# Kernel tuning notes

Measured on AMD Instinct MI355X. Metric: run time of the kernel, lower is better.

Reference implementation:

```python
import jax, jax.numpy as jnp
import numpy as np

B = 16384          # batch
NS = 26            # sparse features
ND = 13            # dense features
V = 100000         # vocab per sparse feature
E = 16             # embedding size
H = 400            # dnn hidden
DNN_IN = NS * E + ND  # 429


def setup_inputs() -> dict:
    key = jax.random.key(0)
    ks = jax.random.split(key, 12)
    X_sparse = jax.random.randint(ks[0], (B, NS), 0, V, dtype=jnp.int32)
    X_dense = jax.random.normal(ks[1], (B, ND), dtype=jnp.float32)
    # stacked per-feature embedding tables: [NS, V, dim]
    emb1 = jax.random.normal(ks[2], (NS, V, 1), dtype=jnp.float32) * 1e-4
    emb2 = jax.random.normal(ks[3], (NS, V, E), dtype=jnp.float32) * 1e-4
    lin_weight = jax.random.normal(ks[4], (ND, 1), dtype=jnp.float32) * 1e-4
    bias = jnp.zeros((1,), dtype=jnp.float32)
    W0 = jax.random.normal(ks[5], (DNN_IN, H), dtype=jnp.float32) * 1e-4
    b0 = jnp.zeros((H,), dtype=jnp.float32)
    W1 = jax.random.normal(ks[6], (H, H), dtype=jnp.float32) * 1e-4
    b1 = jnp.zeros((H,), dtype=jnp.float32)
    W2 = jax.random.normal(ks[7], (H, H), dtype=jnp.float32) * 1e-4
    b2 = jnp.zeros((H,), dtype=jnp.float32)
    W_out = jax.random.normal(ks[8], (H, 1), dtype=jnp.float32) * 1e-4
    return {"X_sparse": X_sparse, "X_dense": X_dense, "emb1": emb1, "emb2": emb2,
            "lin_weight": lin_weight, "bias": bias, "W0": W0, "b0": b0,
            "W1": W1, "b1": b1, "W2": W2, "b2": b2, "W_out": W_out}


def reference(X_sparse, X_dense, emb1, emb2, lin_weight, bias, W0, b0, W1, b1, W2, b2, W_out):
    fidx = jnp.arange(NS)[None, :]            # [1, NS] feature indices
    # ---- FM linear term ----
    e1 = emb1[fidx, X_sparse][..., 0]          # [B, NS] per-feature scalar embeddings
    linear_sparse = jnp.sum(e1, axis=-1, keepdims=True)            # [B, 1]
    linear_dense = X_dense @ lin_weight                            # [B, 1]
    logit = linear_sparse + linear_dense
    # ---- FM second-order cross term ----
    e2 = emb2[fidx, X_sparse]                  # [B, NS, E]
    square_of_sum = jnp.square(jnp.sum(e2, axis=1))                # [B, E]
    sum_of_square = jnp.sum(jnp.square(e2), axis=1)                # [B, E]
    cross = 0.5 * jnp.sum(square_of_sum - sum_of_square, axis=-1, keepdims=True)
    logit = logit + cross
    # ---- DNN (dropout p=0 -> identity) ----
    dnn_in = jnp.concatenate([e2.reshape(e2.shape[0], -1), X_dense], axis=-1)  # [B, 429]
    h = jax.nn.relu(dnn_in @ W0 + b0)
    h = jax.nn.relu(h @ W1 + b1)
    h = jax.nn.relu(h @ W2 + b2)
    logit = logit + h @ W_out
    return logit + bias
```

## Files before the change

kernel.cpp:

```cpp
#include <hip/hip_runtime.h>
#include <hip/hip_bf16.h>

#define B_     16384
#define NS_    26
#define ND_    13
#define V_     100000
#define H_     400
#define NP     448
#define MT     64
#define ASTR   456
#define WCHB   (448 * 64)

#define ACT_OFF   0
#define WBUF_OFF  (MT * ASTR)
#define FMV_OFF   (WBUF_OFF + 2 * WCHB)
#define DOT_OFF   (FMV_OFF + 256)
#define LDSB      (DOT_OFF + 256)

#define SC_A1   2097152.0f
#define SC_A2   2147483648.0f
#define SC_F0   0.125f
#define SC_F1   0.25f
#define SC_G    1.1368683772161603e-13f

typedef float f32x4 __attribute__((ext_vector_type(4)));

__device__ __forceinline__ unsigned char f2fp8(float v) {
  int pk = __builtin_amdgcn_cvt_pk_fp8_f32(v, v, 0, false);
  return (unsigned char)(pk & 0xff);
}

__global__ __launch_bounds__(256) void prep_w(
    const float* __restrict__ W0, const float* __restrict__ W1,
    const float* __restrict__ W2, const float* __restrict__ b0,
    const float* __restrict__ b1, const float* __restrict__ b2,
    const float* __restrict__ Wout,
    unsigned char* __restrict__ W0t, unsigned char* __restrict__ W1t,
    unsigned char* __restrict__ W2t, float* __restrict__ b0p,
    float* __restrict__ b1p, float* __restrict__ b2p,
    float* __restrict__ woutp) {
  const int blk = blockIdx.x;
  const int tid = threadIdx.x;
  if (blk < 147) {
    const int layer = blk / 49;
    const int t = blk - layer * 49;
    const int k0 = (t / 7) * 64, n0 = (t - (t / 7) * 7) * 64;
    const float* W = (layer == 0) ? W0 : (layer == 1) ? W1 : W2;
    unsigned char* Wt = (layer == 0) ? W0t : (layer == 1) ? W1t : W2t;
    const int Kdim = (layer == 0) ? 429 : 400;
    __shared__ float tile[64][65];
#pragma unroll
    for (int p = 0; p < 16; ++p) {
      int kk = p * 4 + (tid >> 6);
      int k = k0 + kk;
      int n = n0 + (tid & 63);
      float v = (k < Kdim && n < H_) ? W[k * H_ + n] : 0.f;
      tile[kk][tid & 63] = v;
    }
    __syncthreads();
#pragma unroll
    for (int p = 0; p < 4; ++p) {
      int nn = p * 16 + (tid >> 4);
      int n = n0 + nn;
      int k4 = (tid & 15) * 4;
      float sc[4];
#pragma unroll
      for (int i = 0; i < 4; ++i) {
        int kabs = k0 + k4 + i;
        sc[i] = (layer == 0 && kabs >= 416) ? 262144.0f : 4096.0f;
      }
      float v0 = tile[k4 + 0][nn] * sc[0];
      float v1 = tile[k4 + 1][nn] * sc[1];
      float v2 = tile[k4 + 2][nn] * sc[2];
      float v3 = tile[k4 + 3][nn] * sc[3];
      int w = __builtin_amdgcn_cvt_pk_fp8_f32(v0, v1, 0, false);
      w = __builtin_amdgcn_cvt_pk_fp8_f32(v2, v3, w, true);
      *(unsigned int*)(Wt + (size_t)n * NP + k0 + k4) = (unsigned int)w;
    }
  } else {
    for (int it = 0; it < 7; ++it) {
      int j = it * 256 + tid;
      if (j < NP)              b0p[j]          = (j < H_) ? b0[j] * SC_A1 : 0.f;
      else if (j < 2 * NP)     b1p[j - NP]     = (j - NP < H_) ? b1[j - NP] * SC_A2 : 0.f;
      else if (j < 3 * NP)     b2p[j - 2*NP]   = (j - 2*NP < H_) ? b2[j - 2*NP] : 0.f;
      else if (j < 4 * NP)     woutp[j - 3*NP] = (j - 3*NP < H_) ? Wout[j - 3*NP] : 0.f;
    }
  }
}

__device__ __forceinline__ void stage_w_chunk(
    const unsigned char* __restrict__ Wt, int kt, unsigned char* wb,
    int wave, int lane) {
#pragma unroll
  for (int i = 0; i < 7; ++i) {
    int sbase = i * 256 + wave * 64;
    int s = sbase + lane;
    int n = s >> 2, g = s & 3;
    const unsigned char* gp = Wt + (size_t)n * NP + kt * 64 + g * 16;
    unsigned char* lp = wb + (size_t)sbase * 16;
    __builtin_amdgcn_global_load_lds(
        (const __attribute__((address_space(1))) unsigned int*)gp,
        (__attribute__((address_space(3))) unsigned int*)lp, 16, 0, 0);
  }
}

__global__ __launch_bounds__(256, 1) void fused_all(
    const int* __restrict__ Xs, const float* __restrict__ Xd,
    const float* __restrict__ emb1, const float* __restrict__ emb2,
    const float* __restrict__ linw, const float* __restrict__ bias,
    const unsigned char* __restrict__ W0t, const unsigned char* __restrict__ W1t,
    const unsigned char* __restrict__ W2t,
    const float* __restrict__ b0p, const float* __restrict__ b1p,
    const float* __restrict__ b2p, const float* __restrict__ woutp,
    float* __restrict__ out) {
  extern __shared__ char smem[];
  unsigned char* act  = (unsigned char*)(smem + ACT_OFF);
  unsigned char* wbuf = (unsigned char*)(smem + WBUF_OFF);
  float* fmv  = (float*)(smem + FMV_OFF);
  float* dotv = (float*)(smem + DOT_OFF);

  const int tid  = threadIdx.x;
  const int wave = tid >> 6;
  const int lane = tid & 63;
  const int quad = lane >> 4;
  const int l16  = lane & 15;
  const int r0   = blockIdx.x * MT;

  stage_w_chunk(W0t, 0, wbuf, wave, lane);

  {
    if (tid < 64) dotv[tid] = 0.f;
    const int r   = lane >> 2;
    const int t4  = lane & 3;
    const int row = wave * 16 + r;
    const int gr  = r0 + row;
    const int* xs = Xs + gr * NS_;

    f32x4 sum = {0.f, 0.f, 0.f, 0.f}, sq = {0.f, 0.f, 0.f, 0.f};
#pragma unroll
    for (int f = 0; f < NS_; ++f) {
      int idx = xs[f];
      f32x4 v = *(const f32x4*)(emb2 + ((size_t)f * V_ + idx) * 16 + t4 * 4);
      sum += v;
      sq  += v * v;
      int pk = __builtin_amdgcn_cvt_pk_fp8_f32(v[0] * 4096.f, v[1] * 4096.f, 0, false);
      pk = __builtin_amdgcn_cvt_pk_fp8_f32(v[2] * 4096.f, v[3] * 4096.f, pk, true);
      *(unsigned int*)(act + row * ASTR + f * 16 + t4 * 4) = (unsigned int)pk;
    }

    float lin = 0.f;
    for (int f = t4; f < NS_; f += 4)
      lin += emb1[(size_t)f * V_ + xs[f]];

    for (int e = 416 + t4; e < NP; e += 4) act[row * ASTR + e] = 0;
    for (int e = t4; e < ND_; e += 4) {
      float xd = Xd[gr * ND_ + e];
      lin += xd * linw[e];
      act[row * ASTR + 416 + e] = f2fp8(xd * 64.f);
    }

    f32x4 c4 = sum * sum - sq;
    float fm = 0.5f * (c4[0] + c4[1] + c4[2] + c4[3]) + lin;
    fm += __shfl_xor(fm, 1, 64);
    fm += __shfl_xor(fm, 2, 64);
    if (t4 == 0) fmv[row] = fm + bias[0];
  }

  const unsigned char* Wl[3] = {W0t, W1t, W2t};

  for (int layer = 0; layer < 3; ++layer) {
    f32x4 acc[4][7] = {};

    for (int kt = 0; kt < 7; ++kt) {
      __syncthreads();
      if (kt < 6)
        stage_w_chunk(Wl[layer], kt + 1, wbuf + ((kt + 1) & 1) * WCHB, wave, lane);
      const unsigned char* wb = wbuf + (kt & 1) * WCHB;

#pragma unroll
      for (int h = 0; h < 2; ++h) {
        long long av[4];
#pragma unroll
        for (int mt = 0; mt < 4; ++mt)
          av[mt] = *(const long long*)(act + (mt * 16 + l16) * ASTR + kt * 64 + h * 32 + quad * 8);
#pragma unroll
        for (int nt = 0; nt < 7; ++nt) {
          long long bv = *(const long long*)(wb + (wave * 112 + nt * 16 + l16) * 64 + h * 32 + quad * 8);
#pragma unroll
          for (int mt = 0; mt < 4; ++mt)
            acc[mt][nt] = __builtin_amdgcn_mfma_f32_16x16x32_fp8_fp8(av[mt], bv, acc[mt][nt], 0, 0, 0);
        }
      }
    }

    __syncthreads();

    if (layer < 2) {
      stage_w_chunk(Wl[layer + 1], 0, wbuf, wave, lane);
      const float fs = (layer == 0) ? SC_F0 : SC_F1;
      const float* bl = (layer == 0) ? b0p : b1p;
#pragma unroll
      for (int nt = 0; nt < 7; ++nt) {
        int col = wave * 112 + nt * 16 + l16;
        float bz = bl[col];
#pragma unroll
        for (int mt = 0; mt < 4; ++mt) {
#pragma unroll
          for (int r = 0; r < 4; ++r) {
            float v = acc[mt][nt][r] * fs + bz;
            v = v > 0.f ? v : 0.f;
            act[(mt * 16 + quad * 4 + r) * ASTR + col] = f2fp8(v);
          }
        }
      }
    } else {
      float wsum[4][4] = {};
#pragma unroll
      for (int nt = 0; nt < 7; ++nt) {
        int col = wave * 112 + nt * 16 + l16;
        float bz = b2p[col];
        float wv = woutp[col];
#pragma unroll
        for (int mt = 0; mt < 4; ++mt) {
#pragma unroll
          for (int r = 0; r < 4; ++r) {
            float v = acc[mt][nt][r] * SC_G + bz;
            v = v > 0.f ? v : 0.f;
            wsum[mt][r] += v * wv;
          }
        }
      }
#pragma unroll
      for (int mt = 0; mt < 4; ++mt) {
#pragma unroll
        for (int r = 0; r < 4; ++r) {
          float s = wsum[mt][r];
          s += __shfl_xor(s, 1, 64);
          s += __shfl_xor(s, 2, 64);
          s += __shfl_xor(s, 4, 64);
          s += __shfl_xor(s, 8, 64);
          if (l16 == 0) atomicAdd(&dotv[mt * 16 + quad * 4 + r], s);
        }
      }
    }
  }

  __syncthreads();
  if (tid < 64) out[r0 + tid] = fmv[tid] + dotv[tid];
}

extern "C" void kernel_launch(void* const* d_in, const int* in_sizes, int n_in,
                              void* d_out, int out_size, void* d_ws, size_t ws_size,
                              hipStream_t stream) {
  const int*   Xs   = (const int*)d_in[0];
  const float* Xd   = (const float*)d_in[1];
  const float* emb1 = (const float*)d_in[2];
  const float* emb2 = (const float*)d_in[3];
  const float* linw = (const float*)d_in[4];
  const float* bias = (const float*)d_in[5];
  const float* W0   = (const float*)d_in[6];
  const float* b0   = (const float*)d_in[7];
  const float* W1   = (const float*)d_in[8];
  const float* b1   = (const float*)d_in[9];
  const float* W2   = (const float*)d_in[10];
  const float* b2   = (const float*)d_in[11];
  const float* Wout = (const float*)d_in[12];
  float* out = (float*)d_out;

  char* ws = (char*)d_ws;
  const size_t WSZ = (size_t)NP * NP;
  unsigned char* W0t = (unsigned char*)(ws);
  unsigned char* W1t = (unsigned char*)(ws + WSZ);
  unsigned char* W2t = (unsigned char*)(ws + 2 * WSZ);
  float* b0p   = (float*)(ws + 3 * WSZ);
  float* b1p   = (float*)(ws + 3 * WSZ + 1792);
  float* b2p   = (float*)(ws + 3 * WSZ + 2 * 1792);
  float* woutp = (float*)(ws + 3 * WSZ + 3 * 1792);

  (void)hipFuncSetAttribute((const void*)fused_all,
                            hipFuncAttributeMaxDynamicSharedMemorySize, LDSB);

  prep_w<<<148, 256, 0, stream>>>(W0, W1, W2, b0, b1, b2, Wout,
                                  W0t, W1t, W2t, b0p, b1p, b2p, woutp);

  fused_all<<<B_ / MT, 256, LDSB, stream>>>(
      Xs, Xd, emb1, emb2, linw, bias, W0t, W1t, W2t,
      b0p, b1p, b2p, woutp, out);
}
```

Measured before the change: 284.5 us.

## Make weight staging wave-private with swizzled LDS layout and vmcnt waits

Each wave now stages only its own 112-column slice of the weight chunk into LDS, so the per-k-tile block-wide __syncthreads is replaced by s_waitcnt on vmcnt within the wave. The LDS layout of weight rows is XOR-swizzled in 16-byte groups to cut bank conflicts on the B-operand reads. Prefetch of the next layer's first chunk is issued before the layer barrier, and barriers are added around the activation rewrite. The correctness of the hard-coded waitcnt encodings and the assumption that no wave reads another's weight slice are the main risks.

After: 274.3 us. 1.04x faster.

```diff
diff --git a/kernel.cpp b/kernel.cpp
--- a/kernel.cpp
+++ b/kernel.cpp
@@ -10,12 +10,16 @@
 #define MT     64
 #define ASTR   456
 #define WCHB   (448 * 64)
+#define WQTR   (112 * 64)
 
 #define ACT_OFF   0
 #define WBUF_OFF  (MT * ASTR)
 #define FMV_OFF   (WBUF_OFF + 2 * WCHB)
 #define DOT_OFF   (FMV_OFF + 256)
 #define LDSB      (DOT_OFF + 256)
+
+#define WAIT_VM7  0x0F77
+#define WAIT_VM0  0x0F70
 
 #define SC_A1   2097152.0f
 #define SC_A2   2147483648.0f
@@ -91,13 +95,15 @@
 __device__ __forceinline__ void stage_w_chunk(
     const unsigned char* __restrict__ Wt, int kt, unsigned char* wb,
     int wave, int lane) {
+  const unsigned char* wrow = Wt + (size_t)(wave * 112) * NP + kt * 64;
+  unsigned char* lbase = wb + wave * WQTR;
 #pragma unroll
   for (int i = 0; i < 7; ++i) {
-    int sbase = i * 256 + wave * 64;
-    int s = sbase + lane;
-    int n = s >> 2, g = s & 3;
-    const unsigned char* gp = Wt + (size_t)n * NP + kt * 64 + g * 16;
-    unsigned char* lp = wb + (size_t)sbase * 16;
+    int s = i * 64 + lane;
+    int nl = s >> 2;
+    int g = (s & 3) ^ ((nl >> 1) & 3);
+    const unsigned char* gp = wrow + (size_t)nl * NP + g * 16;
+    unsigned char* lp = lbase + (size_t)(i * 64) * 16;
     __builtin_amdgcn_global_load_lds(
         (const __attribute__((address_space(1))) unsigned int*)gp,
         (__attribute__((address_space(3))) unsigned int*)lp, 16, 0, 0);
@@ -166,16 +172,24 @@
     if (t4 == 0) fmv[row] = fm + bias[0];
   }
 
+  __syncthreads();
+
   const unsigned char* Wl[3] = {W0t, W1t, W2t};
 
   for (int layer = 0; layer < 3; ++layer) {
+    const unsigned char* Wt = Wl[layer];
+    const unsigned char* wq = wbuf + wave * WQTR;
     f32x4 acc[4][7] = {};
 
     for (int kt = 0; kt < 7; ++kt) {
-      __syncthreads();
-      if (kt < 6)
-        stage_w_chunk(Wl[layer], kt + 1, wbuf + ((kt + 1) & 1) * WCHB, wave, lane);
-      const unsigned char* wb = wbuf + (kt & 1) * WCHB;
+      if (kt < 6) {
+        stage_w_chunk(Wt, kt + 1, wbuf + ((kt + 1) & 1) * WCHB, wave, lane);
+        __builtin_amdgcn_s_waitcnt(WAIT_VM7);
+      } else {
+        __builtin_amdgcn_s_waitcnt(WAIT_VM0);
+      }
+      __builtin_amdgcn_sched_barrier(0);
+      const unsigned char* wb = wq + (kt & 1) * WCHB;
 
 #pragma unroll
       for (int h = 0; h < 2; ++h) {
@@ -185,7 +199,9 @@
           av[mt] = *(const long long*)(act + (mt * 16 + l16) * ASTR + kt * 64 + h * 32 + quad * 8);
 #pragma unroll
         for (int nt = 0; nt < 7; ++nt) {
-          long long bv = *(const long long*)(wb + (wave * 112 + nt * 16 + l16) * 64 + h * 32 + quad * 8);
+          int nl = nt * 16 + l16;
+          int sw = (2 * h + (quad >> 1)) ^ ((nl >> 1) & 3);
+          long long bv = *(const long long*)(wb + nl * 64 + sw * 16 + (quad & 1) * 8);
 #pragma unroll
           for (int mt = 0; mt < 4; ++mt)
             acc[mt][nt] = __builtin_amdgcn_mfma_f32_16x16x32_fp8_fp8(av[mt], bv, acc[mt][nt], 0, 0, 0);
@@ -193,10 +209,11 @@
       }
     }
 
+    if (layer < 2) stage_w_chunk(Wl[layer + 1], 0, wbuf, wave, lane);
+
     __syncthreads();
 
     if (layer < 2) {
-      stage_w_chunk(Wl[layer + 1], 0, wbuf, wave, lane);
       const float fs = (layer == 0) ? SC_F0 : SC_F1;
       const float* bl = (layer == 0) ? b0p : b1p;
 #pragma unroll
@@ -243,9 +260,9 @@
         }
       }
     }
+    __syncthreads();
   }
 
-  __syncthreads();
   if (tid < 64) out[r0 + tid] = fmv[tid] + dotv[tid];
 }
 
```
